# Performance work log

Measured on AMD Instinct MI355X. Metric: run time of the kernel, lower is better.

Reference implementation:

```python
import itertools
import jax, jax.numpy as jnp
import numpy as np

IN_CHANNELS = 8
IN_KERNELS = 32
ORDER = 2


def make_weight(in_channels: int, order: int, in_kernels: int) -> jnp.ndarray:
    """Binary selection weight of shape (Kernels, Combinations, Channels).

    Row r of the (Comb, C) map has 1s at the channels of the r-th combination,
    stacked for all combination sizes 1..order, then repeated per kernel.
    Mirrors torch.combinations + scatter construction in _initialize_weights.
    """
    rows = []
    for o in range(1, order + 1):
        for comb in itertools.combinations(range(in_channels), o):
            row = np.zeros(in_channels, dtype=np.float32)
            row[list(comb)] = 1.0
            rows.append(row)
    w = np.stack(rows, axis=0)  # (Comb, C)
    w = np.broadcast_to(w[None], (in_kernels,) + w.shape).copy()  # (K, Comb, C)
    return jnp.asarray(w)


def setup_inputs() -> dict:
    key = jax.random.key(0)
    B, K, C, T = 8, IN_KERNELS, IN_CHANNELS, 512
    x = jax.random.normal(key, (B, K, C, T), dtype=jnp.float32)
    weight = make_weight(IN_CHANNELS, ORDER, IN_KERNELS)
    return {"x": x, "weight": weight}


def reference(x, weight):
    # x: (B, K, C, T); weight: (K, Comb, C) binary selection map.
    # Multiplicative channel mix: broadcast-mul then replace structural zeros
    # (and any exact data zeros, as in the original) with 1 and take the
    # product over the channel axis.
    y = x[:, :, None, :, :] * weight[None, :, :, :, None]  # (B, K, Comb, C, T)
    y = jnp.where(y != 0, y, jnp.float32(1.0))
    return jnp.prod(y, axis=-2)  # (B, K, Comb, T)
```

## Files before the change

kernel.cpp:

```cpp
#include <hip/hip_runtime.h>


#define BDIM 8
#define KDIM 32
#define CDIM 8
#define TDIM 512
#define COMB 36
#define TQ (TDIM / 4)

__global__ __launch_bounds__(TQ) void channelmix_kernel(
    const float* __restrict__ x, float* __restrict__ out) {
    const int bk = blockIdx.x;
    const int tq = threadIdx.x;

    const float4* __restrict__ xin =
        reinterpret_cast<const float4*>(x + (size_t)bk * CDIM * TDIM);
    float4* __restrict__ o =
        reinterpret_cast<float4*>(out + (size_t)bk * COMB * TDIM);

    float4 f[CDIM];
#pragma unroll
    for (int c = 0; c < CDIM; ++c) {
        float4 v = xin[c * TQ + tq];
        v.x = (v.x != 0.0f) ? v.x : 1.0f;
        v.y = (v.y != 0.0f) ? v.y : 1.0f;
        v.z = (v.z != 0.0f) ? v.z : 1.0f;
        v.w = (v.w != 0.0f) ? v.w : 1.0f;
        f[c] = v;
    }

#pragma unroll
    for (int c = 0; c < CDIM; ++c) {
        o[c * TQ + tq] = f[c];
    }

    int r = CDIM;
#pragma unroll
    for (int a = 0; a < CDIM - 1; ++a) {
#pragma unroll
        for (int b = a + 1; b < CDIM; ++b) {
            float4 p;
            p.x = f[a].x * f[b].x;
            p.y = f[a].y * f[b].y;
            p.z = f[a].z * f[b].z;
            p.w = f[a].w * f[b].w;
            o[r * TQ + tq] = p;
            ++r;
        }
    }
}

extern "C" void kernel_launch(void* const* d_in, const int* in_sizes, int n_in,
                              void* d_out, int out_size, void* d_ws, size_t ws_size,
                              hipStream_t stream) {
    const float* x = (const float*)d_in[0];
    float* out = (float*)d_out;

    const int nblocks = BDIM * KDIM;
    channelmix_kernel<<<nblocks, TQ, 0, stream>>>(x, out);
}
```

Baseline: 10.99 us.

## Parallelize over output combinations with one float4 per thread

```diff
diff --git a/kernel.cpp b/kernel.cpp
--- a/kernel.cpp
+++ b/kernel.cpp
@@ -1,53 +1,51 @@
 #include <hip/hip_runtime.h>
 
 
-#define BDIM 8
-#define KDIM 32
 #define CDIM 8
 #define TDIM 512
 #define COMB 36
 #define TQ (TDIM / 4)
+#define ITEMS (COMB * TQ)
 
-__global__ __launch_bounds__(TQ) void channelmix_kernel(
+__device__ __constant__ unsigned char PA[28] = {
+    0,0,0,0,0,0,0, 1,1,1,1,1,1, 2,2,2,2,2, 3,3,3,3, 4,4,4, 5,5, 6};
+__device__ __constant__ unsigned char PB[28] = {
+    1,2,3,4,5,6,7, 2,3,4,5,6,7, 3,4,5,6,7, 4,5,6,7, 5,6,7, 6,7, 7};
+
+__device__ __forceinline__ float4 fix1(float4 v) {
+    v.x = (v.x != 0.0f) ? v.x : 1.0f;
+    v.y = (v.y != 0.0f) ? v.y : 1.0f;
+    v.z = (v.z != 0.0f) ? v.z : 1.0f;
+    v.w = (v.w != 0.0f) ? v.w : 1.0f;
+    return v;
+}
+
+__global__ __launch_bounds__(256) void channelmix_kernel(
     const float* __restrict__ x, float* __restrict__ out) {
-    const int bk = blockIdx.x;
-    const int tq = threadIdx.x;
+    const int bk = blockIdx.y;
+    const int item = blockIdx.x * 256 + threadIdx.x;
+    const int r = item >> 7;
+    const int tq = item & (TQ - 1);
 
     const float4* __restrict__ xin =
         reinterpret_cast<const float4*>(x + (size_t)bk * CDIM * TDIM);
-    float4* __restrict__ o =
-        reinterpret_cast<float4*>(out + (size_t)bk * COMB * TDIM);
 
-    float4 f[CDIM];
-#pragma unroll
-    for (int c = 0; c < CDIM; ++c) {
-        float4 v = xin[c * TQ + tq];
-        v.x = (v.x != 0.0f) ? v.x : 1.0f;
-        v.y = (v.y != 0.0f) ? v.y : 1.0f;
-        v.z = (v.z != 0.0f) ? v.z : 1.0f;
-        v.w = (v.w != 0.0f) ? v.w : 1.0f;
-        f[c] = v;
+    float4 v;
+    if (r < CDIM) {
+        v = fix1(xin[r * TQ + tq]);
+    } else {
+        const int p = r - CDIM;
+        const int a = PA[p];
+        const int b = PB[p];
+        float4 fa = fix1(xin[a * TQ + tq]);
+        float4 fb = fix1(xin[b * TQ + tq]);
+        v.x = fa.x * fb.x;
+        v.y = fa.y * fb.y;
+        v.z = fa.z * fb.z;
+        v.w = fa.w * fb.w;
     }
 
-#pragma unroll
-    for (int c = 0; c < CDIM; ++c) {
-        o[c * TQ + tq] = f[c];
-    }
-
-    int r = CDIM;
-#pragma unroll
-    for (int a = 0; a < CDIM - 1; ++a) {
-#pragma unroll
-        for (int b = a + 1; b < CDIM; ++b) {
-            float4 p;
-            p.x = f[a].x * f[b].x;
-            p.y = f[a].y * f[b].y;
-            p.z = f[a].z * f[b].z;
-            p.w = f[a].w * f[b].w;
-            o[r * TQ + tq] = p;
-            ++r;
-        }
-    }
+    reinterpret_cast<float4*>(out + (size_t)bk * COMB * TDIM)[r * TQ + tq] = v;
 }
 
 extern "C" void kernel_launch(void* const* d_in, const int* in_sizes, int n_in,
@@ -56,6 +54,6 @@
     const float* x = (const float*)d_in[0];
     float* out = (float*)d_out;
 
-    const int nblocks = BDIM * KDIM;
-    channelmix_kernel<<<nblocks, TQ, 0, stream>>>(x, out);
+    dim3 grid(ITEMS / 256, 256);
+    channelmix_kernel<<<grid, 256, 0, stream>>>(x, out);
 }
```

Result: slower. 11.48 us (+4.5%).
